# Kernel optimization log

Measured on AMD Instinct MI355X. Metric: run time of the kernel, lower is better.

Reference implementation:

```python
import jax, jax.numpy as jnp
import numpy as np
import math

D_MODEL = 1024
N_HEAD = 16
D_HEAD = D_MODEL // N_HEAD
INIT_SIZE = 1200  # RelativeSinusoidalPositionalEmbedding init_size
SCALE = 1.0       # scale=False in __init__


def _rel_pos_embed(L, d_head):
    """Replicates RelativeSinusoidalPositionalEmbedding: table over positions
    [-601, 600] (num=init_size+1=1201 rows), padding row 0 zeroed, then gather
    rows for positions arange(-L/2, L/2) + origin_shift (origin_shift=601)."""
    num = INIT_SIZE + 1                      # 1201
    half = d_head // 2
    freq = jnp.exp(jnp.arange(half, dtype=jnp.float32) * (-math.log(10000.0) / (half - 1)))
    pos_vals = jnp.arange(-num // 2, num // 2, dtype=jnp.float32)   # -601..599 -> 1201 vals
    ang = pos_vals[:, None] * freq[None, :]
    table = jnp.concatenate([jnp.sin(ang), jnp.cos(ang)], axis=1)   # [num, d_head]
    table = table.at[0].set(0.0)             # padding_idx = 0
    origin_shift = num // 2 + 1              # 601
    idx = jnp.arange(-(L // 2), L // 2) + origin_shift   # L even -> L indices
    return table[idx]                        # [L, d_head]


def setup_inputs() -> dict:
    key = jax.random.key(0)
    k1, k2, k3, k4, k5 = jax.random.split(key, 5)
    B, L = 4, 1024
    embed = jax.random.normal(k1, (B, L, D_MODEL), dtype=jnp.float32)
    umask = jnp.ones((B, L), dtype=jnp.int32)                       # 1 = valid utterance
    qmask = jax.random.randint(k2, (B, L), 0, 2).astype(jnp.int64)  # speaker ids {0,1}
    W_qkv = jax.random.normal(k3, (D_MODEL, 4 * D_MODEL), dtype=jnp.float32) * 0.02
    W_pos = jax.random.normal(k4, (D_HEAD, 3 * D_MODEL), dtype=jnp.float32) * 0.02
    W_fc  = jax.random.normal(k5, (D_MODEL, D_MODEL), dtype=jnp.float32) * 0.02
    return {"embed": embed, "umask": umask, "qmask": qmask,
            "W_qkv": W_qkv, "W_pos": W_pos, "W_fc": W_fc}


def reference(embed, umask, qmask, W_qkv, W_pos, W_fc):
    B, L, d = embed.shape
    H, dh = N_HEAD, d // N_HEAD

    # qkv projection and head split
    q, k1, k2, v = jnp.split(embed @ W_qkv, 4, axis=-1)             # each [B, L, d]
    q  = q.reshape(B, L, H, dh).transpose(0, 2, 1, 3)               # [B, H, L, dh]
    k1 = k1.reshape(B, L, H, dh).transpose(0, 2, 1, 3)
    k2 = k2.reshape(B, L, H, dh).transpose(0, 2, 1, 3)
    v  = v.reshape(B, L, H, dh).transpose(0, 2, 1, 3)

    # relative position projections (detached sinusoids -> qk_pos linear)
    pe = _rel_pos_embed(L, dh)                                      # [L, dh]
    qp, kp1, kp2 = jnp.split(pe @ W_pos, 3, axis=-1)                # each [L, d]
    qp  = qp.reshape(L, H, dh).transpose(1, 0, 2)                   # [H, L, dh]
    kp1 = kp1.reshape(L, H, dh).transpose(1, 0, 2)
    kp2 = kp2.reshape(L, H, dh).transpose(1, 0, 2)

    pos1 = jnp.einsum('hqd,hkd->hqk', qp, kp1)                      # [H, L, L]
    pos2 = jnp.einsum('hqd,hkd->hqk', qp, kp2)

    attn_self  = jnp.einsum('bhqd,bhkd->bhqk', q, k1) + pos1[None]  # [B, H, L, L]
    attn_other = jnp.einsum('bhqd,bhkd->bhqk', q, k2) + pos2[None]

    # same-speaker mask: self-attn only where speakers match, other-attn where they differ
    qeq = (qmask[:, :, None] == qmask[:, None, :])                  # [B, L, L] bool
    attn_self  = jnp.where(qeq[:, None], attn_self, 0.0)
    attn_other = jnp.where(qeq[:, None], 0.0, attn_other)
    attn_add = (attn_self + attn_other) / SCALE

    # causal (order) mask + padding mask (eval-mode path of the module)
    order = jnp.triu(jnp.ones((L, L), dtype=bool), 1)[None] | (umask == 0)[:, None, :]
    attn = jnp.where(order[:, None], -jnp.inf, attn_add)
    p = jax.nn.softmax(attn, axis=-1)                               # dropout is identity in eval

    out = jnp.einsum('bhqk,bhkd->bhqd', p, v)                       # [B, H, L, dh]
    out = out.transpose(0, 2, 1, 3).reshape(B, L, d)
    return out @ W_fc
```

## Files before the change

### kernel.cpp

```cpp
#include <hip/hip_runtime.h>
#include <math.h>

#define NB 4
#define SEQ 1024
#define DMODEL 1024
#define NHEAD 16
#define DHEAD 64

typedef __attribute__((ext_vector_type(8))) short s16x8;
typedef __attribute__((ext_vector_type(4))) short s16x4;
typedef __attribute__((ext_vector_type(4))) float f32x4;

__device__ __forceinline__ short f2bf(float f) {
    union { float f; unsigned u; } x; x.f = f;
    unsigned r = x.u + 0x7fffu + ((x.u >> 16) & 1u);
    return (short)(r >> 16);
}

__device__ __forceinline__ unsigned cvtpk(float lo, float hi) {
    unsigned r;
    asm("v_cvt_pk_bf16_f32 %0, %1, %2" : "=v"(r) : "v"(lo), "v"(hi));
    return r;
}

__device__ __forceinline__ f32x4 mfma16(s16x8 a, s16x8 b, f32x4 c) {
    return __builtin_amdgcn_mfma_f32_16x16x32_bf16(a, b, c, 0, 0, 0);
}

__device__ __forceinline__ s16x8 cvt8(float4 a, float4 b) {
    s16x8 v;
    v[0] = f2bf(a.x); v[1] = f2bf(a.y); v[2] = f2bf(a.z); v[3] = f2bf(a.w);
    v[4] = f2bf(b.x); v[5] = f2bf(b.y); v[6] = f2bf(b.z); v[7] = f2bf(b.w);
    return v;
}

__device__ __forceinline__ s16x8 ldlds(const short* base, int byteoff) {
    return *(const s16x8*)((const char*)base + byteoff);
}

#define GLDS16(g, l) __builtin_amdgcn_global_load_lds( \
    (const __attribute__((address_space(1))) unsigned int*)(g), \
    (__attribute__((address_space(3))) unsigned int*)(l), 16, 0, 0)
#define GLDS4(g, l) __builtin_amdgcn_global_load_lds( \
    (const __attribute__((address_space(1))) unsigned int*)(g), \
    (__attribute__((address_space(3))) unsigned int*)(l), 4, 0, 0)

__global__ __launch_bounds__(256) void mask_pack_kernel(
    const int* __restrict__ qmask, const int* __restrict__ umask,
    int* __restrict__ PM)
{
    int b = blockIdx.x;
    for (int k = threadIdx.x; k < 1088; k += 256) {
        int v = 2;
        if (k < 1024)
            v = (qmask[b * 1024 + k] & 1) | ((umask[b * 1024 + k] == 0) ? 2 : 0);
        PM[b * 1088 + k] = v;
    }
}

__global__ __launch_bounds__(256) void convert_embed_kernel(
    const float* __restrict__ src, short* __restrict__ dst)
{
    int i = (blockIdx.x * 256 + threadIdx.x) * 8;
    float4 a = *(const float4*)(src + i);
    float4 b = *(const float4*)(src + i + 4);
    *(s16x8*)(dst + i) = cvt8(a, b);
}

__global__ __launch_bounds__(256) void transpose_w_kernel(
    const float* __restrict__ W, short* __restrict__ WT, int N)
{
    __shared__ short T[64][72];
    int nt = blockIdx.x * 64, kt = blockIdx.y * 64;
    int tid = threadIdx.x;
    int kl = tid >> 4;
    int nl = (tid & 15) * 4;
    #pragma unroll
    for (int rr = 0; rr < 4; ++rr) {
        int k = kl + rr * 16;
        float4 v = *(const float4*)(W + (size_t)(kt + k) * N + nt + nl);
        T[nl + 0][k] = f2bf(v.x);
        T[nl + 1][k] = f2bf(v.y);
        T[nl + 2][k] = f2bf(v.z);
        T[nl + 3][k] = f2bf(v.w);
    }
    __syncthreads();
    int nr = tid >> 2;
    int kc = (tid & 3) * 16;
    uint4 a = *(const uint4*)&T[nr][kc];
    uint4 b = *(const uint4*)&T[nr][kc + 8];
    short* dst = WT + (size_t)(nt + nr) * 1024 + kt + kc;
    *(uint4*)(dst) = a;
    *(uint4*)(dst + 8) = b;
}

__global__ __launch_bounds__(256) void pos_proj_kernel(
    const float* __restrict__ Wpos, short* __restrict__ qpb,
    short* __restrict__ k1cat, short* __restrict__ k2cat)
{
    int bid = blockIdx.x;
    int s = bid >> 7;
    int l0 = (bid & 127) * 8;
    int tid = threadIdx.x;
    __shared__ float pe[8][64];

    for (int idx = tid; idx < 512; idx += 256) {
        int li = idx >> 6, t = idx & 63;
        float p = (float)(l0 + li - 512);
        int j = (t < 32) ? t : (t - 32);
        float f = expf(-0.2971077539f * (float)j);
        float a = p * f;
        pe[li][t] = (t < 32) ? sinf(a) : cosf(a);
    }
    __syncthreads();

    float acc[4][8] = {};
    const float* wp = Wpos + s * 1024 + tid;
    for (int t = 0; t < 64; ++t) {
        float w0 = wp[t * 3072];
        float w1 = wp[t * 3072 + 256];
        float w2 = wp[t * 3072 + 512];
        float w3 = wp[t * 3072 + 768];
        #pragma unroll
        for (int li = 0; li < 8; ++li) {
            float pv = pe[li][t];
            acc[0][li] += pv * w0; acc[1][li] += pv * w1;
            acc[2][li] += pv * w2; acc[3][li] += pv * w3;
        }
    }
    #pragma unroll
    for (int cc = 0; cc < 4; ++cc) {
        int c = tid + cc * 256;
        int h = c >> 6, d = c & 63;
        #pragma unroll
        for (int li = 0; li < 8; ++li) {
            short bv = f2bf(acc[cc][li]);
            if (s == 0) {
                qpb[((size_t)(h << 10) + l0 + li) * 64 + d] = bv;
            } else {
                short* dst = (s == 1) ? k1cat : k2cat;
                #pragma unroll
                for (int bb = 0; bb < 4; ++bb)
                    dst[((size_t)((bb * 16 + h) * 1024) + l0 + li) * 128 + 64 + d] = bv;
            }
        }
    }
}

template<int EPI, int NCOLS>
__global__ __launch_bounds__(256) void gemm_nt(
    const short* __restrict__ A, const short* __restrict__ BT,
    short* __restrict__ o0, short* __restrict__ o1, short* __restrict__ o2,
    short* __restrict__ o3, float* __restrict__ of)
{
    __shared__ short As[128 * 32];
    __shared__ short Bs[128 * 32];

    int nwg = gridDim.x * gridDim.y;
    int lin = blockIdx.y * gridDim.x + blockIdx.x;
    int cpx = nwg >> 3;
    int swb = (lin & 7) * cpx + (lin >> 3);
    int bx = swb % gridDim.x, by = swb / gridDim.x;
    int m0 = by * 128, n0 = bx * 128;

    int tid = threadIdx.x;
    int w = tid >> 6, lane = tid & 63;
    int wm = w >> 1, wn = w & 1;
    int lq = lane & 15, lg = lane >> 4;

    f32x4 zero = {0.f, 0.f, 0.f, 0.f};
    f32x4 acc[4][4];
    #pragma unroll
    for (int i = 0; i < 4; ++i)
        #pragma unroll
        for (int j = 0; j < 4; ++j) acc[i][j] = zero;

    int swz = (((lane & 3) ^ ((lane >> 2) & 3)) << 3);
    int srow = lane >> 2;
    const short* aBase = A  + (size_t)(m0 + (w << 5) + srow) * 1024 + swz;
    const short* bBase = BT + (size_t)(n0 + (w << 5) + srow) * 1024 + swz;
    short* aDst = As + w * 1024;
    short* bDst = Bs + w * 1024;

    for (int kt = 0; kt < 1024; kt += 32) {
        __syncthreads();
        GLDS16(aBase + kt, aDst);
        GLDS16(aBase + kt + 16 * 1024, aDst + 512);
        GLDS16(bBase + kt, bDst);
        GLDS16(bBase + kt + 16 * 1024, bDst + 512);
        __syncthreads();

        s16x8 af[4], bfr[4];
        #pragma unroll
        for (int mt = 0; mt < 4; ++mt) {
            int row = wm * 64 + mt * 16 + lq;
            af[mt] = ldlds(As, (row * 64 + lg * 16) ^ ((row & 3) << 4));
        }
        #pragma unroll
        for (int nt = 0; nt < 4; ++nt) {
            int row = wn * 64 + nt * 16 + lq;
            bfr[nt] = ldlds(Bs, (row * 64 + lg * 16) ^ ((row & 3) << 4));
        }
        #pragma unroll
        for (int mt = 0; mt < 4; ++mt)
            #pragma unroll
            for (int nt = 0; nt < 4; ++nt)
                acc[mt][nt] = mfma16(af[mt], bfr[nt], acc[mt][nt]);
    }

    #pragma unroll
    for (int nt = 0; nt < 4; ++nt) {
        int n = n0 + wn * 64 + nt * 16 + lq;
        int sec = n >> 10, hd = n & 1023;
        int hh = hd >> 6, d = hd & 63;
        #pragma unroll
        for (int mt = 0; mt < 4; ++mt) {
            int mb = m0 + wm * 64 + mt * 16 + lg * 4;
            if constexpr (EPI == 1) {
                #pragma unroll
                for (int r = 0; r < 4; ++r)
                    of[(size_t)(mb + r) * NCOLS + n] = acc[mt][nt][r];
            } else {
                int b = mb >> 10, li0 = mb & 1023;
                int bh = b * 16 + hh;
                if (sec == 3) {
                    s16x4 pv;
                    #pragma unroll
                    for (int r = 0; r < 4; ++r) pv[r] = f2bf(acc[mt][nt][r]);
                    *(s16x4*)(o3 + (((size_t)(bh * 64 + d)) << 10) + li0) = pv;
                } else {
                    #pragma unroll
                    for (int r = 0; r < 4; ++r) {
                        short bv = f2bf(acc[mt][nt][r]);
                        if (sec == 0)
                            o0[((size_t)(bh << 10) + li0 + r) * 64 + d] = bv;
                        else if (sec == 1)
                            o1[((size_t)bh * 1024 + li0 + r) * 128 + d] = bv;
                        else
                            o2[((size_t)bh * 1024 + li0 + r) * 128 + d] = bv;
                    }
                }
            }
        }
    }
}

__global__ __launch_bounds__(256) void attn_kernel(
    const short* __restrict__ qb, const short* __restrict__ k1cat,
    const short* __restrict__ k2cat, const short* __restrict__ vtb,
    const short* __restrict__ qpb, const int* __restrict__ PM,
    const int* __restrict__ qmask, short* __restrict__ ctx)
{
    __shared__ short K1s[2][32 * 128];
    __shared__ short K2s[2][32 * 128];
    __shared__ short Vs[2][64 * 32];
    __shared__ int   PMs[2][64];

    int bid = blockIdx.x;
    int xg = bid & 7, jj = bid >> 3;
    int bh = xg * 8 + (jj & 7);
    int pair = jj >> 3;
    int b = bh >> 4, h = bh & 15;

    int w = threadIdx.x >> 6, lane = threadIdx.x & 63;
    int lq = lane & 15, lg = lane >> 4;

    auto STAGE = [&](int d, int K0) {
        #pragma unroll
        for (int i = 0; i < 5; ++i) {
            int g = w * 5 + i;
            if (g < 8) {
                int row = g * 4 + (lane >> 4);
                int colb = ((lane & 15) << 4) ^ ((row & 7) << 4);
                const short* src = k1cat + ((size_t)bh * 1024 + K0 + row) * 128 + (colb >> 1);
                GLDS16(src, &K1s[d][g * 512]);
            } else if (g < 16) {
                int gg = g - 8;
                int row = gg * 4 + (lane >> 4);
                int colb = ((lane & 15) << 4) ^ ((row & 7) << 4);
                const short* src = k2cat + ((size_t)bh * 1024 + K0 + row) * 128 + (colb >> 1);
                GLDS16(src, &K2s[d][gg * 512]);
            } else {
                int c = g - 16;
                int row = c * 16 + (lane >> 2);
                int colb = ((lane & 3) << 4) ^ ((row & 3) << 4);
                const short* src = vtb + ((size_t)bh * 64 + row) * 1024 + K0 + (colb >> 1);
                GLDS16(src, &Vs[d][c * 512]);
            }
        }
        if (w == 0) {
            GLDS4(PM + b * 1088 + K0 + lane, &PMs[d][0]);
        }
    };

    f32x4 zero = {0.f, 0.f, 0.f, 0.f};

    #pragma unroll 1
    for (int phase = 0; phase < 2; ++phase) {
        int qt = phase ? (15 - pair) : pair;
        int q0 = qt * 64 + w * 16;
        int q_glob = q0 + lq;

        const short* qrow  = qb  + ((size_t)bh * SEQ + q_glob) * DHEAD;
        const short* qprow = qpb + ((size_t)h  * SEQ + q_glob) * DHEAD;
        s16x8 qf0  = *(const s16x8*)(qrow + lg * 8);
        s16x8 qf1  = *(const s16x8*)(qrow + 32 + lg * 8);
        s16x8 qpf0 = *(const s16x8*)(qprow + lg * 8);
        s16x8 qpf1 = *(const s16x8*)(qprow + 32 + lg * 8);
        int qm_q = qmask[b * SEQ + q_glob] & 1;
        asm volatile("s_waitcnt vmcnt(0)" ::: "memory");

        f32x4 accO[4];
        #pragma unroll
        for (int i = 0; i < 4; ++i) accO[i] = zero;
        float m_run = -1e30f, l_run = 0.f;

        int nslab = 2 * qt + 2;
        STAGE(0, 0);

        for (int t = 0; t < nslab; ++t) {
            int cur = t & 1;
            if (t + 1 < nslab) {
                STAGE(cur ^ 1, (t + 1) * 32);
                if (w == 0) asm volatile("s_waitcnt vmcnt(6)" ::: "memory");
                else        asm volatile("s_waitcnt vmcnt(5)" ::: "memory");
            } else {
                asm volatile("s_waitcnt vmcnt(0)" ::: "memory");
            }
            __builtin_amdgcn_s_barrier();
            asm volatile("" ::: "memory");

            int K0 = t * 32;
            if (K0 <= q0 + 15) {
                const short* b1 = K1s[cur];
                const short* b2 = K2s[cur];

                f32x4 s1v[2], s2v[2];
                __builtin_amdgcn_s_setprio(1);
                #pragma unroll
                for (int hh = 0; hh < 2; ++hh) {
                    int row = hh * 16 + lq;
                    int ro = row * 256 + (lg << 4);
                    int sw = (row & 7) << 4;
                    f32x4 tv = zero, uv = zero;
                    tv = mfma16(ldlds(b1, (ro      ) ^ sw), qf0,  tv);
                    tv = mfma16(ldlds(b1, (ro +  64) ^ sw), qf1,  tv);
                    tv = mfma16(ldlds(b1, (ro + 128) ^ sw), qpf0, tv);
                    tv = mfma16(ldlds(b1, (ro + 192) ^ sw), qpf1, tv);
                    s1v[hh] = tv;
                    uv = mfma16(ldlds(b2, (ro      ) ^ sw), qf0,  uv);
                    uv = mfma16(ldlds(b2, (ro +  64) ^ sw), qf1,  uv);
                    uv = mfma16(ldlds(b2, (ro + 128) ^ sw), qpf0, uv);
                    uv = mfma16(ldlds(b2, (ro + 192) ^ sw), qpf1, uv);
                    s2v[hh] = uv;
                }
                __builtin_amdgcn_s_setprio(0);

                float sv[8];
                #pragma unroll
                for (int i = 0; i < 8; ++i) {
                    int hh = i >> 2, r = i & 3;
                    int kl = hh * 16 + lg * 4 + r;
                    int k_idx = K0 + kl;
                    int pm = PMs[cur][kl];
                    float s = ((pm & 1) == qm_q) ? s1v[hh][r] : s2v[hh][r];
                    if (k_idx > q_glob || (pm & 2)) s = -INFINITY;
                    sv[i] = s;
                }
                float tm = sv[0];
                #pragma unroll
                for (int i = 1; i < 8; ++i) tm = fmaxf(tm, sv[i]);
                tm = fmaxf(tm, __shfl_xor(tm, 16));
                tm = fmaxf(tm, __shfl_xor(tm, 32));

                if (!__all(tm <= m_run + 8.0f)) {
                    float m_new = fmaxf(m_run, tm);
                    float scale = __expf(m_run - m_new);
                    m_run = m_new;
                    l_run *= scale;
                    f32x4 scv;
                    scv[0] = __shfl(scale, lg * 4 + 0);
                    scv[1] = __shfl(scale, lg * 4 + 1);
                    scv[2] = __shfl(scale, lg * 4 + 2);
                    scv[3] = __shfl(scale, lg * 4 + 3);
                    #pragma unroll
                    for (int dt = 0; dt < 4; ++dt) accO[dt] *= scv;
                }

                float p[8]; float ps = 0.f;
                #pragma unroll
                for (int i = 0; i < 8; ++i) { p[i] = __expf(sv[i] - m_run); ps += p[i]; }
                ps += __shfl_xor(ps, 16);
                ps += __shfl_xor(ps, 32);
                l_run += ps;

                unsigned dA0 = cvtpk(p[0], p[1]);
                unsigned dA1 = cvtpk(p[2], p[3]);
                unsigned dB0 = cvtpk(p[4], p[5]);
                unsigned dB1 = cvtpk(p[6], p[7]);
                int sl0 = lq + ((lg & 1) << 5);
                int sl1 = sl0 + 16;
                unsigned a0 = (unsigned)__shfl((int)dA0, sl0), a1 = (unsigned)__shfl((int)dA1, sl0);
                unsigned a2 = (unsigned)__shfl((int)dA0, sl1), a3 = (unsigned)__shfl((int)dA1, sl1);
                unsigned c0 = (unsigned)__shfl((int)dB0, sl0), c1 = (unsigned)__shfl((int)dB1, sl0);
                unsigned c2 = (unsigned)__shfl((int)dB0, sl1), c3 = (unsigned)__shfl((int)dB1, sl1);
                bool hi = (lg >= 2);
                union { unsigned u[4]; s16x8 v; } pa;
                pa.u[0] = hi ? c0 : a0; pa.u[1] = hi ? c1 : a1;
                pa.u[2] = hi ? c2 : a2; pa.u[3] = hi ? c3 : a3;

                __builtin_amdgcn_s_setprio(1);
                #pragma unroll
                for (int dt = 0; dt < 4; ++dt) {
                    int vrow = dt * 16 + lq;
                    int voff = (vrow * 64 + (lg << 4)) ^ ((vrow & 3) << 4);
                    accO[dt] = mfma16(pa.v, ldlds(Vs[cur], voff), accO[dt]);
                }
                __builtin_amdgcn_s_setprio(0);
            }

            asm volatile("" ::: "memory");
            __builtin_amdgcn_s_barrier();
        }

        float inv = 1.0f / l_run;
        f32x4 invv;
        invv[0] = __shfl(inv, lg * 4 + 0);
        invv[1] = __shfl(inv, lg * 4 + 1);
        invv[2] = __shfl(inv, lg * 4 + 2);
        invv[3] = __shfl(inv, lg * 4 + 3);
        #pragma unroll
        for (int dt = 0; dt < 4; ++dt) {
            #pragma unroll
            for (int r = 0; r < 4; ++r) {
                int qo = q0 + lg * 4 + r;
                size_t off = ((size_t)(b * SEQ + qo)) * DMODEL + h * DHEAD + dt * 16 + lq;
                ctx[off] = f2bf(accO[dt][r] * invv[r]);
            }
        }
    }
}

extern "C" void kernel_launch(void* const* d_in, const int* in_sizes, int n_in,
                              void* d_out, int out_size, void* d_ws, size_t ws_size,
                              hipStream_t stream) {
    const float* embed = (const float*)d_in[0];
    const int*   umask = (const int*)d_in[1];
    const int*   qmask = (const int*)d_in[2];
    const float* Wqkv  = (const float*)d_in[3];
    const float* Wpos  = (const float*)d_in[4];
    const float* Wfc   = (const float*)d_in[5];
    float* out = (float*)d_out;

    char* w = (char*)d_ws;
    short* qb    = (short*)(w + (0ull  << 20));
    short* vtb   = (short*)(w + (8ull  << 20));
    short* qpb   = (short*)(w + (16ull << 20));
    short* ctx   = (short*)(w + (18ull << 20));
    short* ebf   = ctx;
    short* k1cat = (short*)(w + (26ull << 20));
    short* k2cat = (short*)(w + (42ull << 20));
    int*   PM    = (int*)  (w + (58ull << 20));
    short* WqkvT = (short*)(w + (59ull << 20));
    short* WfcT  = (short*)(w + (67ull << 20));

    hipLaunchKernelGGL(mask_pack_kernel, dim3(4), dim3(256), 0, stream,
                       qmask, umask, PM);
    hipLaunchKernelGGL(pos_proj_kernel, dim3(384), dim3(256), 0, stream,
                       Wpos, qpb, k1cat, k2cat);
    hipLaunchKernelGGL(convert_embed_kernel, dim3(2048), dim3(256), 0, stream,
                       embed, ebf);
    hipLaunchKernelGGL(transpose_w_kernel, dim3(64, 16), dim3(256), 0, stream,
                       Wqkv, WqkvT, 4096);
    hipLaunchKernelGGL(transpose_w_kernel, dim3(16, 16), dim3(256), 0, stream,
                       Wfc, WfcT, 1024);
    hipLaunchKernelGGL((gemm_nt<0, 4096>), dim3(32, 32), dim3(256), 0, stream,
                       ebf, WqkvT, qb, k1cat, k2cat, vtb, (float*)nullptr);
    hipLaunchKernelGGL(attn_kernel, dim3(512), dim3(256), 0, stream,
                       qb, k1cat, k2cat, vtb, qpb, PM, qmask, ctx);
    hipLaunchKernelGGL((gemm_nt<1, 1024>), dim3(8, 32), dim3(256), 0, stream,
                       ctx, WfcT, (short*)nullptr, (short*)nullptr, (short*)nullptr,
                       (short*)nullptr, out);
}
```

Measured before the change: 187.3 us.

## Software-pipeline attention loop: overlap next slab QK with previous slab softmax/PV

Restructures the attention key-slab loop into a two-slab ping-pong. The QK MFMAs, mask loads and V fragment loads for one slab are issued before the softmax and PV MFMAs of the previous slab, so matrix work and the exp/shuffle work can overlap within each wave. V fragments are preloaded into registers so the LDS buffer can be refilled early. This doubles the live score and V registers per wave, which raises register pressure and could lower occupancy.

```diff
diff --git a/kernel.cpp b/kernel.cpp
--- a/kernel.cpp
+++ b/kernel.cpp
@@ -245,6 +245,87 @@
     }
 }
 
+#define QKLOAD(BUF, S1, S2, VF, PMa, PMb) {                                   \
+    const short* b1_ = K1s[BUF];                                              \
+    const short* b2_ = K2s[BUF];                                              \
+    __builtin_amdgcn_s_setprio(1);                                            \
+    for (int hh = 0; hh < 2; ++hh) {                                          \
+        int row_ = hh * 16 + lq;                                              \
+        int ro_ = row_ * 256 + (lg << 4);                                     \
+        int sw_ = (row_ & 7) << 4;                                            \
+        f32x4 tv_ = zero, uv_ = zero;                                         \
+        tv_ = mfma16(ldlds(b1_, (ro_      ) ^ sw_), qf0,  tv_);               \
+        tv_ = mfma16(ldlds(b1_, (ro_ +  64) ^ sw_), qf1,  tv_);               \
+        tv_ = mfma16(ldlds(b1_, (ro_ + 128) ^ sw_), qpf0, tv_);               \
+        tv_ = mfma16(ldlds(b1_, (ro_ + 192) ^ sw_), qpf1, tv_);               \
+        S1[hh] = tv_;                                                         \
+        uv_ = mfma16(ldlds(b2_, (ro_      ) ^ sw_), qf0,  uv_);               \
+        uv_ = mfma16(ldlds(b2_, (ro_ +  64) ^ sw_), qf1,  uv_);               \
+        uv_ = mfma16(ldlds(b2_, (ro_ + 128) ^ sw_), qpf0, uv_);               \
+        uv_ = mfma16(ldlds(b2_, (ro_ + 192) ^ sw_), qpf1, uv_);               \
+        S2[hh] = uv_;                                                         \
+    }                                                                         \
+    __builtin_amdgcn_s_setprio(0);                                            \
+    PMa = *(const int4*)&PMs[BUF][lg * 4];                                    \
+    PMb = *(const int4*)&PMs[BUF][16 + lg * 4];                               \
+    for (int dt = 0; dt < 4; ++dt) VF[dt] = ldlds(Vs[BUF], voffs[dt]);        \
+}
+
+#define FINISH(K0v, S1, S2, VF, PMa, PMb) {                                   \
+    int pme_[8] = {PMa.x, PMa.y, PMa.z, PMa.w, PMb.x, PMb.y, PMb.z, PMb.w};   \
+    float sv_[8];                                                             \
+    for (int i = 0; i < 8; ++i) {                                             \
+        int hh_ = i >> 2, r_ = i & 3;                                         \
+        int k_idx_ = (K0v) + hh_ * 16 + lg * 4 + r_;                          \
+        int pm_ = pme_[i];                                                    \
+        float s_ = ((pm_ & 1) == qm_q) ? S1[hh_][r_] : S2[hh_][r_];           \
+        if (k_idx_ > q_glob || (pm_ & 2)) s_ = -INFINITY;                     \
+        sv_[i] = s_;                                                          \
+    }                                                                         \
+    float tm_ = sv_[0];                                                       \
+    for (int i = 1; i < 8; ++i) tm_ = fmaxf(tm_, sv_[i]);                     \
+    tm_ = fmaxf(tm_, __shfl_xor(tm_, 16));                                    \
+    tm_ = fmaxf(tm_, __shfl_xor(tm_, 32));                                    \
+    if (!__all(tm_ <= m_run + 8.0f)) {                                        \
+        float mn_ = fmaxf(m_run, tm_);                                        \
+        float sc_ = __expf(m_run - mn_);                                      \
+        m_run = mn_; l_run *= sc_;                                            \
+        f32x4 scv_;                                                           \
+        scv_[0] = __shfl(sc_, lg * 4 + 0);                                    \
+        scv_[1] = __shfl(sc_, lg * 4 + 1);                                    \
+        scv_[2] = __shfl(sc_, lg * 4 + 2);                                    \
+        scv_[3] = __shfl(sc_, lg * 4 + 3);                                    \
+        for (int dt = 0; dt < 4; ++dt) accO[dt] *= scv_;                      \
+    }                                                                         \
+    float p_[8]; float ps_ = 0.f;                                             \
+    for (int i = 0; i < 8; ++i) { p_[i] = __expf(sv_[i] - m_run); ps_ += p_[i]; } \
+    ps_ += __shfl_xor(ps_, 16);                                               \
+    ps_ += __shfl_xor(ps_, 32);                                               \
+    l_run += ps_;                                                             \
+    unsigned dA0_ = cvtpk(p_[0], p_[1]);                                      \
+    unsigned dA1_ = cvtpk(p_[2], p_[3]);                                      \
+    unsigned dB0_ = cvtpk(p_[4], p_[5]);                                      \
+    unsigned dB1_ = cvtpk(p_[6], p_[7]);                                      \
+    int sl0_ = lq + ((lg & 1) << 5);                                          \
+    int sl1_ = sl0_ + 16;                                                     \
+    unsigned a0_ = (unsigned)__shfl((int)dA0_, sl0_);                         \
+    unsigned a1_ = (unsigned)__shfl((int)dA1_, sl0_);                         \
+    unsigned a2_ = (unsigned)__shfl((int)dA0_, sl1_);                         \
+    unsigned a3_ = (unsigned)__shfl((int)dA1_, sl1_);                         \
+    unsigned c0_ = (unsigned)__shfl((int)dB0_, sl0_);                         \
+    unsigned c1_ = (unsigned)__shfl((int)dB1_, sl0_);                         \
+    unsigned c2_ = (unsigned)__shfl((int)dB0_, sl1_);                         \
+    unsigned c3_ = (unsigned)__shfl((int)dB1_, sl1_);                         \
+    bool hi_ = (lg >= 2);                                                     \
+    union { unsigned u[4]; s16x8 v; } pa_;                                    \
+    pa_.u[0] = hi_ ? c0_ : a0_; pa_.u[1] = hi_ ? c1_ : a1_;                   \
+    pa_.u[2] = hi_ ? c2_ : a2_; pa_.u[3] = hi_ ? c3_ : a3_;                   \
+    __builtin_amdgcn_s_setprio(1);                                            \
+    for (int dt = 0; dt < 4; ++dt)                                            \
+        accO[dt] = mfma16(pa_.v, VF[dt], accO[dt]);                           \
+    __builtin_amdgcn_s_setprio(0);                                            \
+}
+
 __global__ __launch_bounds__(256) void attn_kernel(
     const short* __restrict__ qb, const short* __restrict__ k1cat,
     const short* __restrict__ k2cat, const short* __restrict__ vtb,
@@ -295,6 +376,13 @@
 
     f32x4 zero = {0.f, 0.f, 0.f, 0.f};
 
+    int voffs[4];
+    #pragma unroll
+    for (int dt = 0; dt < 4; ++dt) {
+        int vrow = dt * 16 + lq;
+        voffs[dt] = (vrow * 64 + (lg << 4)) ^ ((vrow & 3) << 4);
+    }
+
     #pragma unroll 1
     for (int phase = 0; phase < 2; ++phase) {
         int qt = phase ? (15 - pair) : pair;
@@ -316,12 +404,29 @@
         float m_run = -1e30f, l_run = 0.f;
 
         int nslab = 2 * qt + 2;
+
+        f32x4 s1A[2], s2A[2], s1B[2], s2B[2];
+        s16x8 vfA[4], vfB[4];
+        int4 pmA0, pmA1, pmB0, pmB1;
+        bool doA = false, doB = false, pendB = false;
+
         STAGE(0, 0);
 
-        for (int t = 0; t < nslab; ++t) {
-            int cur = t & 1;
-            if (t + 1 < nslab) {
-                STAGE(cur ^ 1, (t + 1) * 32);
+        #pragma unroll 1
+        for (int tt = 0; tt < nslab; tt += 2) {
+            STAGE(1, (tt + 1) * 32);
+            if (w == 0) asm volatile("s_waitcnt vmcnt(6)" ::: "memory");
+            else        asm volatile("s_waitcnt vmcnt(5)" ::: "memory");
+            __builtin_amdgcn_s_barrier();
+            asm volatile("" ::: "memory");
+            doA = (tt * 32 <= q0 + 15);
+            if (doA) QKLOAD(0, s1A, s2A, vfA, pmA0, pmA1);
+            if (pendB) FINISH((tt - 1) * 32, s1B, s2B, vfB, pmB0, pmB1);
+            asm volatile("" ::: "memory");
+            __builtin_amdgcn_s_barrier();
+
+            if (tt + 2 < nslab) {
+                STAGE(0, (tt + 2) * 32);
                 if (w == 0) asm volatile("s_waitcnt vmcnt(6)" ::: "memory");
                 else        asm volatile("s_waitcnt vmcnt(5)" ::: "memory");
             } else {
@@ -329,99 +434,14 @@
             }
             __builtin_amdgcn_s_barrier();
             asm volatile("" ::: "memory");
-
-            int K0 = t * 32;
-            if (K0 <= q0 + 15) {
-                const short* b1 = K1s[cur];
-                const short* b2 = K2s[cur];
-
-                f32x4 s1v[2], s2v[2];
-                __builtin_amdgcn_s_setprio(1);
-                #pragma unroll
-                for (int hh = 0; hh < 2; ++hh) {
-                    int row = hh * 16 + lq;
-                    int ro = row * 256 + (lg << 4);
-                    int sw = (row & 7) << 4;
-                    f32x4 tv = zero, uv = zero;
-                    tv = mfma16(ldlds(b1, (ro      ) ^ sw), qf0,  tv);
-                    tv = mfma16(ldlds(b1, (ro +  64) ^ sw), qf1,  tv);
-                    tv = mfma16(ldlds(b1, (ro + 128) ^ sw), qpf0, tv);
-                    tv = mfma16(ldlds(b1, (ro + 192) ^ sw), qpf1, tv);
-                    s1v[hh] = tv;
-                    uv = mfma16(ldlds(b2, (ro      ) ^ sw), qf0,  uv);
-                    uv = mfma16(ldlds(b2, (ro +  64) ^ sw), qf1,  uv);
-                    uv = mfma16(ldlds(b2, (ro + 128) ^ sw), qpf0, uv);
-                    uv = mfma16(ldlds(b2, (ro + 192) ^ sw), qpf1, uv);
-                    s2v[hh] = uv;
-                }
-                __builtin_amdgcn_s_setprio(0);
-
-                float sv[8];
-                #pragma unroll
-                for (int i = 0; i < 8; ++i) {
-                    int hh = i >> 2, r = i & 3;
-                    int kl = hh * 16 + lg * 4 + r;
-                    int k_idx = K0 + kl;
-                    int pm = PMs[cur][kl];
-                    float s = ((pm & 1) == qm_q) ? s1v[hh][r] : s2v[hh][r];
-                    if (k_idx > q_glob || (pm & 2)) s = -INFINITY;
-                    sv[i] = s;
-                }
-                float tm = sv[0];
-                #pragma unroll
-                for (int i = 1; i < 8; ++i) tm = fmaxf(tm, sv[i]);
-                tm = fmaxf(tm, __shfl_xor(tm, 16));
-                tm = fmaxf(tm, __shfl_xor(tm, 32));
-
-                if (!__all(tm <= m_run + 8.0f)) {
-                    float m_new = fmaxf(m_run, tm);
-                    float scale = __expf(m_run - m_new);
-                    m_run = m_new;
-                    l_run *= scale;
-                    f32x4 scv;
-                    scv[0] = __shfl(scale, lg * 4 + 0);
-                    scv[1] = __shfl(scale, lg * 4 + 1);
-                    scv[2] = __shfl(scale, lg * 4 + 2);
-                    scv[3] = __shfl(scale, lg * 4 + 3);
-                    #pragma unroll
-                    for (int dt = 0; dt < 4; ++dt) accO[dt] *= scv;
-                }
-
-                float p[8]; float ps = 0.f;
-                #pragma unroll
-                for (int i = 0; i < 8; ++i) { p[i] = __expf(sv[i] - m_run); ps += p[i]; }
-                ps += __shfl_xor(ps, 16);
-                ps += __shfl_xor(ps, 32);
-                l_run += ps;
-
-                unsigned dA0 = cvtpk(p[0], p[1]);
-                unsigned dA1 = cvtpk(p[2], p[3]);
-                unsigned dB0 = cvtpk(p[4], p[5]);
-                unsigned dB1 = cvtpk(p[6], p[7]);
-                int sl0 = lq + ((lg & 1) << 5);
-                int sl1 = sl0 + 16;
-                unsigned a0 = (unsigned)__shfl((int)dA0, sl0), a1 = (unsigned)__shfl((int)dA1, sl0);
-                unsigned a2 = (unsigned)__shfl((int)dA0, sl1), a3 = (unsigned)__shfl((int)dA1, sl1);
-                unsigned c0 = (unsigned)__shfl((int)dB0, sl0), c1 = (unsigned)__shfl((int)dB1, sl0);
-                unsigned c2 = (unsigned)__shfl((int)dB0, sl1), c3 = (unsigned)__shfl((int)dB1, sl1);
-                bool hi = (lg >= 2);
-                union { unsigned u[4]; s16x8 v; } pa;
-                pa.u[0] = hi ? c0 : a0; pa.u[1] = hi ? c1 : a1;
-                pa.u[2] = hi ? c2 : a2; pa.u[3] = hi ? c3 : a3;
-
-                __builtin_amdgcn_s_setprio(1);
-                #pragma unroll
-                for (int dt = 0; dt < 4; ++dt) {
-                    int vrow = dt * 16 + lq;
-                    int voff = (vrow * 64 + (lg << 4)) ^ ((vrow & 3) << 4);
-                    accO[dt] = mfma16(pa.v, ldlds(Vs[cur], voff), accO[dt]);
-                }
-                __builtin_amdgcn_s_setprio(0);
-            }
-
+            doB = ((tt + 1) * 32 <= q0 + 15);
+            if (doB) QKLOAD(1, s1B, s2B, vfB, pmB0, pmB1);
+            if (doA) FINISH(tt * 32, s1A, s2A, vfA, pmA0, pmA1);
+            pendB = doB;
             asm volatile("" ::: "memory");
             __builtin_amdgcn_s_barrier();
         }
+        if (pendB) FINISH((nslab - 1) * 32, s1B, s2B, vfB, pmB0, pmB1);
 
         float inv = 1.0f / l_run;
         f32x4 invv;
```

After: 233.5 us. +24.6%, slower.
